# Optimization experiments

Hardware: AMD Instinct MI355X
Metric: run time of the kernel (lower is better)

The kernel has to match this reference:

```python
import jax, jax.numpy as jnp
import numpy as np

BINS = 8
EPS = 1e-12  # torch F.normalize default eps


def _pairwise_scores(matf):
    # torch: input1[a,b]=matf[b]; transpose(0,1)->matf[a]; transpose(-2,-1)->matf[a]^T [M,F]
    # matmul with input1[a,b]=matf[b] -> scores[a,b] = matf[a]^T @ matf[b], shape [M,M]
    bs, F, M = matf.shape
    s = jnp.einsum('afm,bfn->abmn', matf, matf)  # [bs, bs, M, M]
    return s.reshape(bs * bs, M * M)


def _histc_rows(x, bins):
    # torch.histc semantics with min=max=0: range = [row.min(), row.max()],
    # values == max land in the last bin.
    mn = jnp.min(x, axis=1, keepdims=True)
    mx = jnp.max(x, axis=1, keepdims=True)
    denom = jnp.where(mx > mn, mx - mn, jnp.ones_like(mx))
    idx = jnp.clip(jnp.floor((x - mn) / denom * bins).astype(jnp.int32), 0, bins - 1)
    nbs = x.shape[0]
    flat = (idx + (jnp.arange(nbs, dtype=jnp.int32) * bins)[:, None]).ravel()
    h = jnp.zeros(nbs * bins, dtype=x.dtype).at[flat].add(1.0)
    return h.reshape(nbs, bins)


def _l2_normalize(h):
    n = jnp.linalg.norm(h, axis=-1, keepdims=True)
    return h / jnp.maximum(n, EPS)


def setup_inputs() -> dict:
    key = jax.random.key(0)
    k1, k2 = jax.random.split(key)
    bs, F, M = 64, 256, 128
    matf1 = jax.random.normal(k1, (bs, F, M), dtype=jnp.float32)
    matf2 = jax.random.normal(k2, (bs, F, M), dtype=jnp.float32)
    return {"matf1": matf1, "matf2": matf2}


def reference(matf1, matf2):
    # scores are .detach()ed in the original; stop_gradient for faithfulness
    scores1 = jax.lax.stop_gradient(_pairwise_scores(matf1))  # [nbs, M*M]
    scores2 = jax.lax.stop_gradient(_pairwise_scores(matf2))
    h1 = _l2_normalize(_histc_rows(scores1, BINS))  # [nbs, 8]
    h2 = _l2_normalize(_histc_rows(scores2, BINS))
    return jnp.concatenate([h1, h2], axis=-1)  # [nbs, 16]
```

## Files before the change

kernel.cpp:

```cpp
#include <hip/hip_runtime.h>
#include <math.h>

#define BS 64
#define F  256
#define M  128
#define MF (M * F)
#define NBP 1056

typedef unsigned short u16;
typedef _Float16 f16x8 __attribute__((ext_vector_type(8)));
typedef float    f32x16 __attribute__((ext_vector_type(16)));

__global__ __launch_bounds__(256) void convert_f16_kernel(
    const float* __restrict__ m1, const float* __restrict__ m2,
    u16* __restrict__ hT)
{
    __shared__ float tile[64 * M];
    const int mat = blockIdx.x >> 6;
    const int b   = blockIdx.x & 63;
    const int f0  = blockIdx.y * 64;
    const float* src = (mat == 0 ? m1 : m2) + (size_t)b * MF + (size_t)f0 * M;
    const int tid = threadIdx.x;

    const float4* g = (const float4*)src;
    float4* s = (float4*)tile;
    #pragma unroll
    for (int i = 0; i < 8; ++i)
        s[tid + i * 256] = g[tid + i * 256];
    __syncthreads();

    const size_t obase = ((size_t)(mat * BS + b) * 32 + (f0 >> 3)) * 1024;
    #pragma unroll
    for (int it = 0; it < 4; ++it) {
        const int idx = it * 256 + tid;
        const int f8l = idx >> 7;
        const int m   = idx & 127;
        u16 hh[8] __attribute__((aligned(16)));
        #pragma unroll
        for (int j = 0; j < 8; ++j) {
            const float x = tile[(f8l * 8 + j) * M + m];
            const _Float16 h = (_Float16)x;
            hh[j] = __builtin_bit_cast(u16, h);
        }
        *(uint4*)&hT[obase + (size_t)idx * 8] = *(const uint4*)hh;
    }
}

__device__ __forceinline__ void async16(const u16* g, u16* l) {
    __builtin_amdgcn_global_load_lds(
        (const __attribute__((address_space(1))) unsigned int*)g,
        (__attribute__((address_space(3))) unsigned int*)l, 16, 0, 0);
}

__global__ __launch_bounds__(256, 2) void gram_hist_mfma(
    const u16* __restrict__ hT, float* __restrict__ out)
{
    __shared__ u16 lds[2 * 12288];
    __shared__ float smin[4], smax[4];
    __shared__ int hist[2][8];

    const int tid  = threadIdx.x;
    const int lane = tid & 63;
    const int w    = tid >> 6;

    if (tid < 16) hist[tid >> 3][tid & 7] = 0;

    int p = blockIdx.x, a = 0;
    { int cnt = 32; while (p >= cnt) { p -= cnt; ++a; cnt = (64 - a + 1) >> 1; } }
    const int b1 = a + 2 * p;
    int b2 = b1 + 1;
    const bool b2valid = (b2 <= 63);
    if (!b2valid) b2 = b1;
    const int mat = blockIdx.y;

    const u16* Asrc  = hT + (size_t)(mat * BS + a)  * MF;
    const u16* B1src = hT + (size_t)(mat * BS + b1) * MF;
    const u16* B2src = hT + (size_t)(mat * BS + b2) * MF;

    auto stage = [&](int bufo, int k0) {
        const int koff = k0 * 128;
        #pragma unroll
        for (int g = 0; g < 6; ++g) {
            const int idx = (g & 1) * 256 + tid;
            const u16* s = (g < 2 ? Asrc : (g < 4 ? B1src : B2src)) + koff + idx * 8;
            async16(s, &lds[bufo + (g >> 1) * 4096 + idx * 8]);
        }
    };

    const int pp = w >> 1;
    const int c  = w & 1;
    const int l31   = lane & 31;
    const int lhalf = lane >> 5;

    f32x16 acc[4][2];
    #pragma unroll
    for (int ti = 0; ti < 4; ++ti)
        #pragma unroll
        for (int u = 0; u < 2; ++u)
            #pragma unroll
            for (int r = 0; r < 16; ++r) acc[ti][u][r] = 0.0f;

    stage(0, 0);
    __syncthreads();

    for (int it = 0; it < 8; ++it) {
        const int cur = (it & 1) * 12288;
        if (it < 7) stage(cur ^ 12288, (it + 1) * 32);

        #pragma unroll
        for (int kk = 0; kk < 2; ++kk) {
            const int kb = kk * 2 + lhalf;
            f16x8 af[4], bf[2];
            #pragma unroll
            for (int t = 0; t < 4; ++t)
                af[t] = *(const f16x8*)&lds[cur + (kb * 128 + t * 32 + l31) * 8];
            #pragma unroll
            for (int t = 0; t < 2; ++t)
                bf[t] = *(const f16x8*)&lds[cur + (1 + pp) * 4096 + (kb * 128 + c * 64 + t * 32 + l31) * 8];
            #pragma unroll
            for (int ti = 0; ti < 4; ++ti)
                #pragma unroll
                for (int u = 0; u < 2; ++u)
                    acc[ti][u] = __builtin_amdgcn_mfma_f32_32x32x16_f16(af[ti], bf[u], acc[ti][u], 0, 0, 0);
        }
        __syncthreads();
    }

    float vmin = acc[0][0][0], vmax = vmin;
    #pragma unroll
    for (int ti = 0; ti < 4; ++ti)
        #pragma unroll
        for (int u = 0; u < 2; ++u)
            #pragma unroll
            for (int r = 0; r < 16; ++r) {
                vmin = fminf(vmin, acc[ti][u][r]);
                vmax = fmaxf(vmax, acc[ti][u][r]);
            }
    #pragma unroll
    for (int off = 1; off < 64; off <<= 1) {
        vmin = fminf(vmin, __shfl_xor(vmin, off, 64));
        vmax = fmaxf(vmax, __shfl_xor(vmax, off, 64));
    }
    if (lane == 0) { smin[w] = vmin; smax[w] = vmax; }
    __syncthreads();
    const float pmn = fminf(smin[pp * 2], smin[pp * 2 + 1]);
    const float pmx = fmaxf(smax[pp * 2], smax[pp * 2 + 1]);
    const float denom = (pmx > pmn) ? (pmx - pmn) : 1.0f;
    const float scale = 8.0f / denom;
    const float bias  = -pmn * scale;

    unsigned w0 = 0, w1 = 0;
    #pragma unroll
    for (int ti = 0; ti < 4; ++ti)
        #pragma unroll
        for (int u = 0; u < 2; ++u)
            #pragma unroll
            for (int r = 0; r < 16; ++r) {
                const float t = fmaf(acc[ti][u][r], scale, bias);
                int k = (int)t;
                k = k > 7 ? 7 : k;
                const unsigned inc = 1u << ((k & 3) * 8);
                if (k < 4) w0 += inc; else w1 += inc;
            }
    unsigned e0 = (w0 & 0xFFu)         | (((w0 >> 8)  & 0xFFu) << 16);
    unsigned e1 = ((w0 >> 16) & 0xFFu) | (((w0 >> 24) & 0xFFu) << 16);
    unsigned e2 = (w1 & 0xFFu)         | (((w1 >> 8)  & 0xFFu) << 16);
    unsigned e3 = ((w1 >> 16) & 0xFFu) | (((w1 >> 24) & 0xFFu) << 16);
    #pragma unroll
    for (int off = 32; off > 0; off >>= 1) {
        e0 += __shfl_down(e0, off, 64);
        e1 += __shfl_down(e1, off, 64);
        e2 += __shfl_down(e2, off, 64);
        e3 += __shfl_down(e3, off, 64);
    }
    if (lane == 0) {
        atomicAdd(&hist[pp][0], (int)(e0 & 0xFFFFu)); atomicAdd(&hist[pp][1], (int)(e0 >> 16));
        atomicAdd(&hist[pp][2], (int)(e1 & 0xFFFFu)); atomicAdd(&hist[pp][3], (int)(e1 >> 16));
        atomicAdd(&hist[pp][4], (int)(e2 & 0xFFFFu)); atomicAdd(&hist[pp][5], (int)(e2 >> 16));
        atomicAdd(&hist[pp][6], (int)(e3 & 0xFFFFu)); atomicAdd(&hist[pp][7], (int)(e3 >> 16));
    }
    __syncthreads();

    const int B = (pp == 0) ? b1 : b2;
    const bool valid = (pp == 0) || b2valid;
    if (valid && c == 0 && lane < 8) {
        float ss = 0.0f;
        #pragma unroll
        for (int k = 0; k < 8; ++k) {
            const float cc = (float)hist[pp][k];
            ss += cc * cc;
        }
        const float nrm = fmaxf(sqrtf(ss), 1e-12f);
        const float v = (float)hist[pp][lane] / nrm;
        out[((size_t)a * BS + B) * 16 + mat * 8 + lane] = v;
        if (a != B)
            out[((size_t)B * BS + a) * 16 + mat * 8 + lane] = v;
    }
}

extern "C" void kernel_launch(void* const* d_in, const int* in_sizes, int n_in,
                              void* d_out, int out_size, void* d_ws, size_t ws_size,
                              hipStream_t stream) {
    const float* m1 = (const float*)d_in[0];
    const float* m2 = (const float*)d_in[1];
    float* out = (float*)d_out;

    u16* hT = (u16*)d_ws;

    convert_f16_kernel<<<dim3(128, 4), 256, 0, stream>>>(m1, m2, hT);
    gram_hist_mfma<<<dim3(NBP, 2), 256, 0, stream>>>(hT, out);
}
```

Before: 120.7 us.

## Split gram tile across eight waves with 512-thread blocks

Doubles the workgroup to 512 threads so each wave computes a 64x64 sub-tile (2x2 MFMAs) instead of 128x64 (4x2), which halves the accumulator registers per wave. Staging now issues three async loads per thread instead of six, and the min/max reduction combines four waves per pair. The intent is more waves in flight per CU to hide LDS and global latency. The cost is more A-fragment LDS reads per MFMA, since A is reloaded by more waves, plus larger barrier groups.

```diff
diff --git a/kernel.cpp b/kernel.cpp
--- a/kernel.cpp
+++ b/kernel.cpp
@@ -52,11 +52,11 @@
         (__attribute__((address_space(3))) unsigned int*)l, 16, 0, 0);
 }
 
-__global__ __launch_bounds__(256, 2) void gram_hist_mfma(
+__global__ __launch_bounds__(512, 4) void gram_hist_mfma(
     const u16* __restrict__ hT, float* __restrict__ out)
 {
     __shared__ u16 lds[2 * 12288];
-    __shared__ float smin[4], smax[4];
+    __shared__ float smin[8], smax[8];
     __shared__ int hist[2][8];
 
     const int tid  = threadIdx.x;
@@ -73,68 +73,66 @@
     if (!b2valid) b2 = b1;
     const int mat = blockIdx.y;
 
-    const u16* Asrc  = hT + (size_t)(mat * BS + a)  * MF;
-    const u16* B1src = hT + (size_t)(mat * BS + b1) * MF;
-    const u16* B2src = hT + (size_t)(mat * BS + b2) * MF;
-
-    auto stage = [&](int bufo, int k0) {
-        const int koff = k0 * 128;
-        #pragma unroll
-        for (int g = 0; g < 6; ++g) {
-            const int idx = (g & 1) * 256 + tid;
-            const u16* s = (g < 2 ? Asrc : (g < 4 ? B1src : B2src)) + koff + idx * 8;
-            async16(s, &lds[bufo + (g >> 1) * 4096 + idx * 8]);
-        }
+    const u16* srcs[3] = {
+        hT + (size_t)(mat * BS + a)  * MF,
+        hT + (size_t)(mat * BS + b1) * MF,
+        hT + (size_t)(mat * BS + b2) * MF,
     };
 
-    const int pp = w >> 1;
-    const int c  = w & 1;
+    auto stage = [&](int bufo, int koff) {
+        #pragma unroll
+        for (int g = 0; g < 3; ++g)
+            async16(srcs[g] + koff + tid * 8, &lds[bufo + g * 4096 + tid * 8]);
+    };
+
+    const int pp = w >> 2;
+    const int rr = (w >> 1) & 1;
+    const int cc = w & 1;
     const int l31   = lane & 31;
     const int lhalf = lane >> 5;
 
-    f32x16 acc[4][2];
-    #pragma unroll
-    for (int ti = 0; ti < 4; ++ti)
-        #pragma unroll
-        for (int u = 0; u < 2; ++u)
-            #pragma unroll
-            for (int r = 0; r < 16; ++r) acc[ti][u][r] = 0.0f;
+    f32x16 acc[2][2];
+    #pragma unroll
+    for (int ti = 0; ti < 2; ++ti)
+        #pragma unroll
+        for (int tj = 0; tj < 2; ++tj)
+            #pragma unroll
+            for (int r = 0; r < 16; ++r) acc[ti][tj][r] = 0.0f;
 
     stage(0, 0);
     __syncthreads();
 
     for (int it = 0; it < 8; ++it) {
         const int cur = (it & 1) * 12288;
-        if (it < 7) stage(cur ^ 12288, (it + 1) * 32);
+        if (it < 7) stage(cur ^ 12288, (it + 1) * 4096);
 
         #pragma unroll
         for (int kk = 0; kk < 2; ++kk) {
             const int kb = kk * 2 + lhalf;
-            f16x8 af[4], bf[2];
-            #pragma unroll
-            for (int t = 0; t < 4; ++t)
-                af[t] = *(const f16x8*)&lds[cur + (kb * 128 + t * 32 + l31) * 8];
-            #pragma unroll
-            for (int t = 0; t < 2; ++t)
-                bf[t] = *(const f16x8*)&lds[cur + (1 + pp) * 4096 + (kb * 128 + c * 64 + t * 32 + l31) * 8];
-            #pragma unroll
-            for (int ti = 0; ti < 4; ++ti)
+            f16x8 af[2], bf[2];
+            #pragma unroll
+            for (int t = 0; t < 2; ++t) {
+                af[t] = *(const f16x8*)&lds[cur + (kb * 128 + rr * 64 + t * 32 + l31) * 8];
+                bf[t] = *(const f16x8*)&lds[cur + (1 + pp) * 4096 + (kb * 128 + cc * 64 + t * 32 + l31) * 8];
+            }
+            #pragma unroll
+            for (int ti = 0; ti < 2; ++ti)
                 #pragma unroll
-                for (int u = 0; u < 2; ++u)
-                    acc[ti][u] = __builtin_amdgcn_mfma_f32_32x32x16_f16(af[ti], bf[u], acc[ti][u], 0, 0, 0);
+                for (int tj = 0; tj < 2; ++tj)
+                    acc[ti][tj] = __builtin_amdgcn_mfma_f32_32x32x16_f16(af[ti], bf[tj], acc[ti][tj], 0, 0, 0);
         }
         __syncthreads();
     }
 
     float vmin = acc[0][0][0], vmax = vmin;
     #pragma unroll
-    for (int ti = 0; ti < 4; ++ti)
-        #pragma unroll
-        for (int u = 0; u < 2; ++u)
+    for (int ti = 0; ti < 2; ++ti)
+        #pragma unroll
+        for (int tj = 0; tj < 2; ++tj)
             #pragma unroll
             for (int r = 0; r < 16; ++r) {
-                vmin = fminf(vmin, acc[ti][u][r]);
-                vmax = fmaxf(vmax, acc[ti][u][r]);
+                vmin = fminf(vmin, acc[ti][tj][r]);
+                vmax = fmaxf(vmax, acc[ti][tj][r]);
             }
     #pragma unroll
     for (int off = 1; off < 64; off <<= 1) {
@@ -143,20 +141,21 @@
     }
     if (lane == 0) { smin[w] = vmin; smax[w] = vmax; }
     __syncthreads();
-    const float pmn = fminf(smin[pp * 2], smin[pp * 2 + 1]);
-    const float pmx = fmaxf(smax[pp * 2], smax[pp * 2 + 1]);
+    const int hb = pp * 4;
+    const float pmn = fminf(fminf(smin[hb], smin[hb + 1]), fminf(smin[hb + 2], smin[hb + 3]));
+    const float pmx = fmaxf(fmaxf(smax[hb], smax[hb + 1]), fmaxf(smax[hb + 2], smax[hb + 3]));
     const float denom = (pmx > pmn) ? (pmx - pmn) : 1.0f;
     const float scale = 8.0f / denom;
     const float bias  = -pmn * scale;
 
     unsigned w0 = 0, w1 = 0;
     #pragma unroll
-    for (int ti = 0; ti < 4; ++ti)
-        #pragma unroll
-        for (int u = 0; u < 2; ++u)
+    for (int ti = 0; ti < 2; ++ti)
+        #pragma unroll
+        for (int tj = 0; tj < 2; ++tj)
             #pragma unroll
             for (int r = 0; r < 16; ++r) {
-                const float t = fmaf(acc[ti][u][r], scale, bias);
+                const float t = fmaf(acc[ti][tj][r], scale, bias);
                 int k = (int)t;
                 k = k > 7 ? 7 : k;
                 const unsigned inc = 1u << ((k & 3) * 8);
@@ -183,12 +182,12 @@
 
     const int B = (pp == 0) ? b1 : b2;
     const bool valid = (pp == 0) || b2valid;
-    if (valid && c == 0 && lane < 8) {
+    if (valid && rr == 0 && cc == 0 && lane < 8) {
         float ss = 0.0f;
         #pragma unroll
         for (int k = 0; k < 8; ++k) {
-            const float cc = (float)hist[pp][k];
-            ss += cc * cc;
+            const float c = (float)hist[pp][k];
+            ss += c * c;
         }
         const float nrm = fmaxf(sqrtf(ss), 1e-12f);
         const float v = (float)hist[pp][lane] / nrm;
@@ -208,5 +207,5 @@
     u16* hT = (u16*)d_ws;
 
     convert_f16_kernel<<<dim3(128, 4), 256, 0, stream>>>(m1, m2, hT);
-    gram_hist_mfma<<<dim3(NBP, 2), 256, 0, stream>>>(hT, out);
-}
+    gram_hist_mfma<<<dim3(NBP, 2), 512, 0, stream>>>(hT, out);
+}
```

Measured after the change: 120.7 us. Within noise of the previous version (-0.0%).

## Load MFMA fragments directly from global memory and swizzle block order for locality

Applied to the files above, without the earlier changes.

Removes the LDS double-buffered async staging and the per-iteration barriers. Each wave now loads its f16x8 fragments straight from global memory with a fully unrolled 16-step K loop. Block indices are also remapped with an interleaved ordering (bx&7)*132+(bx>>3), likely to spread blocks across XCDs so that blocks sharing an A matrix hit the same L2. The cost is that loads are no longer shared through LDS across waves, which raises L2/global traffic, and the removed pipelining may expose memory latency.

```diff
diff --git a/kernel.cpp b/kernel.cpp
--- a/kernel.cpp
+++ b/kernel.cpp
@@ -46,16 +46,9 @@
     }
 }
 
-__device__ __forceinline__ void async16(const u16* g, u16* l) {
-    __builtin_amdgcn_global_load_lds(
-        (const __attribute__((address_space(1))) unsigned int*)g,
-        (__attribute__((address_space(3))) unsigned int*)l, 16, 0, 0);
-}
-
 __global__ __launch_bounds__(256, 2) void gram_hist_mfma(
     const u16* __restrict__ hT, float* __restrict__ out)
 {
-    __shared__ u16 lds[2 * 12288];
     __shared__ float smin[4], smax[4];
     __shared__ int hist[2][8];
 
@@ -65,7 +58,9 @@
 
     if (tid < 16) hist[tid >> 3][tid & 7] = 0;
 
-    int p = blockIdx.x, a = 0;
+    const int bx = blockIdx.x;
+    int p = (bx & 7) * 132 + (bx >> 3);
+    int a = 0;
     { int cnt = 32; while (p >= cnt) { p -= cnt; ++a; cnt = (64 - a + 1) >> 1; } }
     const int b1 = a + 2 * p;
     int b2 = b1 + 1;
@@ -73,24 +68,16 @@
     if (!b2valid) b2 = b1;
     const int mat = blockIdx.y;
 
-    const u16* Asrc  = hT + (size_t)(mat * BS + a)  * MF;
-    const u16* B1src = hT + (size_t)(mat * BS + b1) * MF;
-    const u16* B2src = hT + (size_t)(mat * BS + b2) * MF;
-
-    auto stage = [&](int bufo, int k0) {
-        const int koff = k0 * 128;
-        #pragma unroll
-        for (int g = 0; g < 6; ++g) {
-            const int idx = (g & 1) * 256 + tid;
-            const u16* s = (g < 2 ? Asrc : (g < 4 ? B1src : B2src)) + koff + idx * 8;
-            async16(s, &lds[bufo + (g >> 1) * 4096 + idx * 8]);
-        }
-    };
-
     const int pp = w >> 1;
     const int c  = w & 1;
     const int l31   = lane & 31;
     const int lhalf = lane >> 5;
+
+    const u16* Abase = hT + (size_t)(mat * BS + a) * MF;
+    const u16* Bbase = hT + (size_t)(mat * BS + (pp == 0 ? b1 : b2)) * MF;
+
+    const u16* pa = Abase + lhalf * 1024 + l31 * 8;
+    const u16* pb = Bbase + lhalf * 1024 + (c * 64 + l31) * 8;
 
     f32x16 acc[4][2];
     #pragma unroll
@@ -100,30 +87,23 @@
             #pragma unroll
             for (int r = 0; r < 16; ++r) acc[ti][u][r] = 0.0f;
 
-    stage(0, 0);
-    __syncthreads();
-
-    for (int it = 0; it < 8; ++it) {
-        const int cur = (it & 1) * 12288;
-        if (it < 7) stage(cur ^ 12288, (it + 1) * 32);
-
-        #pragma unroll
-        for (int kk = 0; kk < 2; ++kk) {
-            const int kb = kk * 2 + lhalf;
-            f16x8 af[4], bf[2];
-            #pragma unroll
-            for (int t = 0; t < 4; ++t)
-                af[t] = *(const f16x8*)&lds[cur + (kb * 128 + t * 32 + l31) * 8];
-            #pragma unroll
-            for (int t = 0; t < 2; ++t)
-                bf[t] = *(const f16x8*)&lds[cur + (1 + pp) * 4096 + (kb * 128 + c * 64 + t * 32 + l31) * 8];
-            #pragma unroll
-            for (int ti = 0; ti < 4; ++ti)
-                #pragma unroll
-                for (int u = 0; u < 2; ++u)
-                    acc[ti][u] = __builtin_amdgcn_mfma_f32_32x32x16_f16(af[ti], bf[u], acc[ti][u], 0, 0, 0);
-        }
-        __syncthreads();
+    #pragma unroll
+    for (int kk = 0; kk < 16; ++kk) {
+        const int ko = kk * 2048;
+        const f16x8 a0 = *(const f16x8*)(pa + ko);
+        const f16x8 a1 = *(const f16x8*)(pa + ko + 256);
+        const f16x8 a2 = *(const f16x8*)(pa + ko + 512);
+        const f16x8 a3 = *(const f16x8*)(pa + ko + 768);
+        const f16x8 b0 = *(const f16x8*)(pb + ko);
+        const f16x8 b1f = *(const f16x8*)(pb + ko + 256);
+        acc[0][0] = __builtin_amdgcn_mfma_f32_32x32x16_f16(a0, b0,  acc[0][0], 0, 0, 0);
+        acc[0][1] = __builtin_amdgcn_mfma_f32_32x32x16_f16(a0, b1f, acc[0][1], 0, 0, 0);
+        acc[1][0] = __builtin_amdgcn_mfma_f32_32x32x16_f16(a1, b0,  acc[1][0], 0, 0, 0);
+        acc[1][1] = __builtin_amdgcn_mfma_f32_32x32x16_f16(a1, b1f, acc[1][1], 0, 0, 0);
+        acc[2][0] = __builtin_amdgcn_mfma_f32_32x32x16_f16(a2, b0,  acc[2][0], 0, 0, 0);
+        acc[2][1] = __builtin_amdgcn_mfma_f32_32x32x16_f16(a2, b1f, acc[2][1], 0, 0, 0);
+        acc[3][0] = __builtin_amdgcn_mfma_f32_32x32x16_f16(a3, b0,  acc[3][0], 0, 0, 0);
+        acc[3][1] = __builtin_amdgcn_mfma_f32_32x32x16_f16(a3, b1f, acc[3][1], 0, 0, 0);
     }
 
     float vmin = acc[0][0][0], vmax = vmin;
```

Result: slower. 124.3 us (+3.0%).
